# Optimization experiments

Measured on AMD Instinct MI355X. Metric: run time of the kernel, lower is better.

Reference implementation:

```python
import jax, jax.numpy as jnp
import numpy as np

N = 100000   # nodes
E = 3200000  # edges (avg degree 32)
G = 512      # graphs in batch
F_IN = 10
H = 30


def setup_inputs() -> dict:
    key = jax.random.key(0)
    ks = jax.random.split(key, 14)
    x = jax.random.normal(ks[0], (N, F_IN), dtype=jnp.float32)
    edge_index = jax.random.randint(ks[1], (2, E), 0, N, dtype=jnp.int64)
    batch = jnp.sort(jax.random.randint(ks[2], (N,), 0, G, dtype=jnp.int64))
    edge_weights = jnp.ones((E,), dtype=jnp.float32)
    s = 0.1
    W1 = jax.random.normal(ks[3], (F_IN, H), jnp.float32) * s
    b1 = jnp.zeros((H,), jnp.float32)
    W2 = jax.random.normal(ks[4], (H, H), jnp.float32) * s
    b2 = jnp.zeros((H,), jnp.float32)
    W3 = jax.random.normal(ks[5], (H, H), jnp.float32) * s
    b3 = jnp.zeros((H,), jnp.float32)
    LW1 = jax.random.normal(ks[6], (H, 10), jnp.float32) * s
    Lb1 = jnp.zeros((10,), jnp.float32)
    LW2 = jax.random.normal(ks[7], (10, 2), jnp.float32) * s
    Lb2 = jnp.zeros((2,), jnp.float32)
    return dict(x=x, edge_index=edge_index, batch=batch, edge_weights=edge_weights,
                W1=W1, b1=b1, W2=W2, b2=b2, W3=W3, b3=b3,
                LW1=LW1, Lb1=Lb1, LW2=LW2, Lb2=Lb2)


def reference(x, edge_index, batch, edge_weights, W1, b1, W2, b2, W3, b3, LW1, Lb1, LW2, Lb2):
    n = x.shape[0]
    row, col = edge_index[0], edge_index[1]
    # PyG gcn_norm: add self-loops with weight 1, symmetric normalization
    loop = jnp.arange(n)
    row_f = jnp.concatenate([row, loop])
    col_f = jnp.concatenate([col, loop])
    w_f = jnp.concatenate([edge_weights, jnp.ones((n,), edge_weights.dtype)])
    deg = jax.ops.segment_sum(w_f, col_f, num_segments=n)
    dis = jnp.where(deg > 0, jax.lax.rsqrt(jnp.where(deg > 0, deg, 1.0)), 0.0)
    norm = dis[row_f] * w_f * dis[col_f]  # [E+N]

    def gcn(h, W, b):
        h = h @ W  # [N, out]
        agg = jax.ops.segment_sum(norm[:, None] * h[row_f], col_f, num_segments=n)
        return agg + b

    h = jax.nn.relu(gcn(x, W1, b1))
    h = jax.nn.relu(gcn(h, W2, b2))
    h = jax.nn.relu(gcn(h, W3, b3))  # embedding [N, 30]
    pooled = jax.ops.segment_max(h, batch, num_segments=G)  # [G, 30]
    out = jax.nn.relu(pooled @ LW1 + Lb1) @ LW2 + Lb2  # [G, 2]
    return out
```

## Files before the change

kernel.cpp:

```cpp
#include <hip/hip_runtime.h>
#include <hip/hip_bf16.h>


#define WG 256
#define CAP 9216
#define T_EDGES 16384

__global__ void k_init(int* bcur, float* pooled, int nb16, int pooledN) {
    int i = blockIdx.x * blockDim.x + threadIdx.x;
    if (i < nb16) bcur[i] = 0;
    if (i < pooledN) pooled[i] = 0.0f;
}

__global__ __launch_bounds__(1024)
void k_bucket(const int* __restrict__ row, const int* __restrict__ col,
              const float* __restrict__ w,
              int* bcur, int2* __restrict__ buck, int E, int NB) {
    __shared__ int hist[512];
    __shared__ int base[512];
    int tid = threadIdx.x;
    for (int i = tid; i < NB; i += 1024) hist[i] = 0;
    __syncthreads();
    int start = blockIdx.x * T_EDGES;
    int end = min(start + T_EDGES, E);
    for (int i = start + tid; i < end; i += 1024)
        atomicAdd(&hist[col[i] >> 8], 1);
    __syncthreads();
    for (int i = tid; i < NB; i += 1024) {
        int h = hist[i];
        base[i] = (h > 0) ? atomicAdd(&bcur[i * 16], h) : 0;
        hist[i] = 0;
    }
    __syncthreads();
    for (int i = start + tid; i < end; i += 1024) {
        int c = col[i];
        int b = c >> 8;
        int off = atomicAdd(&hist[b], 1);
        int pos = base[b] + off;
        if (pos < CAP) {
            int2 pk;
            pk.x = (c & 255) | (row[i] << 8);
            pk.y = __float_as_int(w[i]);
            buck[(size_t)b * CAP + pos] = pk;
        }
    }
}

__global__ __launch_bounds__(1024)
void k_fuse(const int* __restrict__ bcur, const int2* __restrict__ buck,
            const float* __restrict__ x,
            float* __restrict__ dis, int* __restrict__ ptr,
            int2* __restrict__ csr, float* __restrict__ xp, int N, int NB) {
    __shared__ int lc[256];
    __shared__ float lw[256];
    __shared__ int sh[256];
    __shared__ int cur[256];
    __shared__ int sb[512];
    __shared__ float ds[256];
    int b = blockIdx.x;
    int tid = threadIdx.x;
    if (tid < 512) sb[tid] = (tid < NB) ? min(bcur[tid * 16], CAP) : 0;
    if (tid < 256) { lc[tid] = 0; lw[tid] = 0.0f; }
    __syncthreads();
    for (int off = 1; off < 512; off <<= 1) {
        int v = (tid < 512 && tid >= off) ? sb[tid - off] : 0;
        __syncthreads();
        if (tid < 512) sb[tid] += v;
        __syncthreads();
    }
    int m = min(bcur[b * 16], CAP);
    int bbase = sb[b] - m;
    if (b == 0 && tid == 0) ptr[N] = sb[511];
    const int2* bp = buck + (size_t)b * CAP;
    for (int i = tid; i < m; i += 1024) {
        int2 pk = bp[i];
        int lcol = pk.x & 255;
        atomicAdd(&lc[lcol], 1);
        atomicAdd(&lw[lcol], __int_as_float(pk.y));
    }
    __syncthreads();
    int lcnt = 0;
    if (tid < 256) { lcnt = lc[tid]; sh[tid] = lcnt; }
    __syncthreads();
    for (int off = 1; off < 256; off <<= 1) {
        int t = (tid >= off && tid < 256) ? sh[tid - off] : 0;
        __syncthreads();
        if (tid < 256) sh[tid] += t;
        __syncthreads();
    }
    int node = (b << 8) + tid;
    if (tid < 256) {
        int base = bbase + sh[tid] - lcnt;
        cur[tid] = base;
        float d = 1.0f + lw[tid];
        float dv = (d > 0.0f) ? (1.0f / sqrtf(d)) : 0.0f;
        ds[tid] = dv;
        if (node < N) {
            ptr[node] = base;
            dis[node] = dv;
        }
    }
    __syncthreads();
    for (int i = tid; i < m; i += 1024) {
        int2 pk = bp[i];
        int lcol = pk.x & 255;
        int pos = atomicAdd(&cur[lcol], 1);
        int2 rec;
        rec.x = (int)(((unsigned)pk.x) >> 8);
        rec.y = pk.y;
        csr[pos] = rec;
    }
    for (int i = tid; i < 256 * 16; i += 1024) {
        int nl = i >> 4, f = i & 15;
        int nd = (b << 8) + nl;
        if (nd < N)
            xp[(size_t)nd * 16 + f] = (f < 10) ? ds[nl] * x[(size_t)nd * 10 + f] : 0.0f;
    }
}

__global__ void k_agg16(const float* __restrict__ xp, const float* __restrict__ dis,
                        const int* __restrict__ ptr, const int2* __restrict__ csr,
                        float* __restrict__ y, int n) {
    int wid = (blockIdx.x * blockDim.x + threadIdx.x) >> 6;
    int lane = threadIdx.x & 63;
    if (wid >= n) return;
    int f = lane & 15;
    int q = lane >> 4;
    int s = ptr[wid];
    int e = ptr[wid + 1];
    float acc = 0.0f;
    int i = s;
    int efull = s + ((e - s) & ~31);
    for (; i < efull; i += 32) {
        int idxv = 0; float nrmv = 0.0f;
        if (lane < 32) {
            int2 v = csr[i + lane];
            idxv = v.x;
            nrmv = __int_as_float(v.y);
        }
#pragma unroll
        for (int j = 0; j < 8; j++) {
            int sl = 4 * j + q;
            int r = __shfl(idxv, sl, 64);
            float w = __shfl(nrmv, sl, 64);
            acc += w * xp[(size_t)r * 16 + f];
        }
    }
    int rem = e - i;
    if (rem > 0) {
        int idxv = 0; float nrmv = 0.0f;
        if (lane < rem) {
            int2 v = csr[i + lane];
            idxv = v.x;
            nrmv = __int_as_float(v.y);
        }
        for (int t = 0; t < rem; t += 8) {
#pragma unroll
            for (int j = 0; j < 2; j++) {
                int sl = t + 4 * j + q;
                int r = __shfl(idxv, sl, 64);
                float w = __shfl(nrmv, sl, 64);
                acc += w * xp[(size_t)r * 16 + f];
            }
        }
    }
    acc += __shfl_xor(acc, 16, 64);
    acc += __shfl_xor(acc, 32, 64);
    float dc = dis[wid];
    float r = dc * (acc + xp[(size_t)wid * 16 + f]);
    if (lane < 16) y[(size_t)wid * 16 + f] = r;
}

__global__ __launch_bounds__(256)
void k_lin1(const float* __restrict__ y, const float* __restrict__ W1,
            const float* __restrict__ b1, const float* __restrict__ W2,
            const float* __restrict__ dis, float* __restrict__ out, int n) {
    __shared__ float W1s[10 * 32];
    __shared__ float W2s[30 * 32];
    __shared__ float b1s[32];
    __shared__ float ys[8][16];
    __shared__ float hs[8][32];
    int tid = threadIdx.x;
    for (int i = tid; i < 10 * 32; i += 256) { int k = i >> 5, f = i & 31; W1s[i] = (f < 30) ? W1[k * 30 + f] : 0.0f; }
    for (int i = tid; i < 30 * 32; i += 256) { int k = i >> 5, f = i & 31; W2s[i] = (f < 30) ? W2[k * 30 + f] : 0.0f; }
    if (tid < 32) b1s[tid] = (tid < 30) ? b1[tid] : 0.0f;
    int n8 = tid >> 5, f = tid & 31;
    int node = blockIdx.x * 8 + n8;
    __syncthreads();
    if (node < n && f < 16) ys[n8][f] = y[(size_t)node * 16 + f];
    __syncthreads();
    if (node < n) {
        float h = b1s[f];
#pragma unroll
        for (int k = 0; k < 10; k++) h += ys[n8][k] * W1s[k * 32 + f];
        h = fmaxf(h, 0.0f);
        if (f >= 30) h = 0.0f;
        hs[n8][f] = h;
    }
    __syncthreads();
    if (node < n) {
        float o = 0.0f;
#pragma unroll
        for (int k = 0; k < 30; k++) o += hs[n8][k] * W2s[k * 32 + f];
        out[(size_t)node * 32 + f] = o * dis[node];
    }
}

__global__ void k_matmul30(const float* __restrict__ in,
                           const float* __restrict__ W, const float* __restrict__ dis,
                           float* __restrict__ out, int n) {
    __shared__ float Ws[30 * 30];
    for (int idx = threadIdx.x; idx < 30 * 30; idx += blockDim.x) Ws[idx] = W[idx];
    __syncthreads();
    int gid = blockIdx.x * blockDim.x + threadIdx.x;
    int node = gid >> 5;
    int f = gid & 31;
    if (node < n) {
        float acc = 0.0f;
        if (f < 30) {
            const float* ip = in + (size_t)node * 32;
#pragma unroll
            for (int k = 0; k < 30; k++) acc += ip[k] * Ws[k * 30 + f];
            acc *= dis[node];
        }
        out[(size_t)node * 32 + f] = acc;
    }
}

__global__ void k_agg(const float* __restrict__ hw, const float* __restrict__ dis,
                      const int* __restrict__ ptr, const int2* __restrict__ csr,
                      const float* __restrict__ bias,
                      float* __restrict__ out, int n) {
    int wid = (blockIdx.x * blockDim.x + threadIdx.x) >> 6;
    int lane = threadIdx.x & 63;
    if (wid >= n) return;
    int f = lane & 31;
    int half = lane >> 5;
    int s = ptr[wid];
    int e = ptr[wid + 1];
    float acc = 0.0f;
    int i = s;
    int efull = s + ((e - s) & ~31);
    for (; i < efull; i += 32) {
        int idxv = 0; float nrmv = 0.0f;
        if (lane < 32) {
            int2 v = csr[i + lane];
            idxv = v.x;
            nrmv = __int_as_float(v.y);
        }
#pragma unroll
        for (int j = 0; j < 16; j++) {
            int sl = 2 * j + half;
            int r = __shfl(idxv, sl, 64);
            float w = __shfl(nrmv, sl, 64);
            acc += w * hw[(size_t)r * 32 + f];
        }
    }
    int rem = e - i;
    if (rem > 0) {
        int idxv = 0; float nrmv = 0.0f;
        if (lane < rem) {
            int2 v = csr[i + lane];
            idxv = v.x;
            nrmv = __int_as_float(v.y);
        }
        for (int t = 0; t < rem; t += 8) {
#pragma unroll
            for (int j = 0; j < 4; j++) {
                int sl = t + 2 * j + half;
                int r = __shfl(idxv, sl, 64);
                float w = __shfl(nrmv, sl, 64);
                acc += w * hw[(size_t)r * 32 + f];
            }
        }
    }
    acc += __shfl_xor(acc, 32, 64);
    float dc = dis[wid];
    float r = dc * (acc + hw[(size_t)wid * 32 + f]);
    if (half == 0 && f < 30) {
        r += bias[f];
        out[(size_t)wid * 32 + f] = fmaxf(r, 0.0f);
    }
}

__global__ void k_pool(const float* __restrict__ h, const int* __restrict__ batch,
                       float* pooled, int n) {
    int gid = blockIdx.x * blockDim.x + threadIdx.x;
    int chunk = gid >> 5;
    int f = gid & 31;
    int n0 = chunk * 64;
    if (n0 >= n || f >= 30) return;
    int end = min(n0 + 64, n);
    int curg = batch[n0];
    float m = 0.0f;
    for (int i = n0; i < end; i++) {
        int g = batch[i];
        if (g != curg) {
            atomicMax((int*)&pooled[curg * 32 + f], __float_as_int(m));
            m = 0.0f;
            curg = g;
        }
        m = fmaxf(m, h[(size_t)i * 32 + f]);
    }
    atomicMax((int*)&pooled[curg * 32 + f], __float_as_int(m));
}

__global__ void k_mlp(const float* __restrict__ pooled,
                      const float* __restrict__ LW1, const float* __restrict__ Lb1,
                      const float* __restrict__ LW2, const float* __restrict__ Lb2,
                      float* __restrict__ out, int G) {
    int g = blockIdx.x * blockDim.x + threadIdx.x;
    if (g >= G) return;
    float p[30];
#pragma unroll
    for (int k = 0; k < 30; k++) p[k] = pooled[g * 32 + k];
    float o0 = Lb2[0], o1 = Lb2[1];
#pragma unroll
    for (int j = 0; j < 10; j++) {
        float hj = Lb1[j];
#pragma unroll
        for (int k = 0; k < 30; k++) hj += p[k] * LW1[k * 10 + j];
        hj = fmaxf(hj, 0.0f);
        o0 += hj * LW2[j * 2 + 0];
        o1 += hj * LW2[j * 2 + 1];
    }
    out[g * 2 + 0] = o0;
    out[g * 2 + 1] = o1;
}

extern "C" void kernel_launch(void* const* d_in, const int* in_sizes, int n_in,
                              void* d_out, int out_size, void* d_ws, size_t ws_size,
                              hipStream_t stream) {
    const float* x     = (const float*)d_in[0];
    const int*   ei    = (const int*)d_in[1];
    const int*   batch = (const int*)d_in[2];
    const float* ew    = (const float*)d_in[3];
    const float* W1 = (const float*)d_in[4];  const float* b1  = (const float*)d_in[5];
    const float* W2 = (const float*)d_in[6];  const float* b2  = (const float*)d_in[7];
    const float* W3 = (const float*)d_in[8];  const float* b3  = (const float*)d_in[9];
    const float* LW1 = (const float*)d_in[10]; const float* Lb1 = (const float*)d_in[11];
    const float* LW2 = (const float*)d_in[12]; const float* Lb2 = (const float*)d_in[13];
    float* out = (float*)d_out;

    const int N = in_sizes[2];
    const int E = in_sizes[3];
    const int G = out_size / 2;
    const int* row = ei;
    const int* col = ei + E;

    const int NB = (N + 255) >> 8;

    char* p = (char*)d_ws;
    auto carve = [&](size_t bytes) -> void* {
        void* r = (void*)p;
        p += (bytes + 255) & ~(size_t)255;
        return r;
    };
    int*   ptr       = (int*)carve((size_t)(N + 1) * 4);
    float* dis       = (float*)carve((size_t)N * 4);
    int*   bcur      = (int*)carve((size_t)NB * 16 * 4);
    float* xp        = (float*)carve((size_t)N * 16 * 4);
    int2*  csr       = (int2*)carve((size_t)E * 8);
    size_t buckBytes = (size_t)NB * CAP * 8;
    size_t featBytes = (size_t)N * 32 * 4 * 2;
    char*  regionA   = (char*)carve(buckBytes > featBytes ? buckBytes : featBytes);
    int2*  buck      = (int2*)regionA;
    float* bufA      = (float*)regionA;
    float* y16       = (float*)regionA;
    float* bufB      = (float*)(regionA + (size_t)N * 32 * 4);
    float* pooled    = (float*)carve((size_t)G * 32 * 4);

    int initN = (NB * 16 > G * 32) ? NB * 16 : G * 32;

    k_init<<<(initN + WG - 1) / WG, WG, 0, stream>>>(bcur, pooled, NB * 16, G * 32);
    k_bucket<<<(E + T_EDGES - 1) / T_EDGES, 1024, 0, stream>>>(row, col, ew, bcur, buck, E, NB);
    k_fuse<<<NB, 1024, 0, stream>>>(bcur, buck, x, dis, ptr, csr, xp, N, NB);

    int agg_grid = (int)(((size_t)N * 64 + WG - 1) / WG);
    int mm_grid  = (int)(((size_t)N * 32 + WG - 1) / WG);

    k_agg16<<<agg_grid, WG, 0, stream>>>(xp, dis, ptr, csr, y16, N);
    k_lin1<<<(N + 7) / 8, 256, 0, stream>>>(y16, W1, b1, W2, dis, bufB, N);
    k_agg<<<agg_grid, WG, 0, stream>>>(bufB, dis, ptr, csr, b2, bufA, N);
    k_matmul30<<<mm_grid, WG, 0, stream>>>(bufA, W3, dis, bufB, N);
    k_agg<<<agg_grid, WG, 0, stream>>>(bufB, dis, ptr, csr, b3, bufA, N);

    int pool_grid = (int)((((size_t)(N + 63) / 64) * 32 + WG - 1) / WG);
    k_pool<<<pool_grid, WG, 0, stream>>>(bufA, batch, pooled, N);
    k_mlp<<<(G + WG - 1) / WG, WG, 0, stream>>>(pooled, LW1, Lb1, LW2, Lb2, out, G);
}
```

Baseline: 429.7 us.

## Use per-wave histograms in edge bucketing and split feature staging into own kernel

The bucketing kernel now keeps a separate shared-memory histogram for each wave and caches column indices in registers. This cuts LDS atomic contention and avoids reloading col in the scatter pass. Per-wave prefix offsets are computed for each bin before the single global atomic reservation. The scaling of x by dis moves out of k_fuse into a separate elementwise kernel, which adds one launch but shortens the fused CSR-build kernel. The register array and the larger shared footprint may reduce occupancy.

```diff
diff --git a/kernel.cpp b/kernel.cpp
--- a/kernel.cpp
+++ b/kernel.cpp
@@ -5,6 +5,7 @@
 #define WG 256
 #define CAP 9216
 #define T_EDGES 16384
+#define NBINS 392
 
 __global__ void k_init(int* bcur, float* pooled, int nb16, int pooledN) {
     int i = blockIdx.x * blockDim.x + threadIdx.x;
@@ -16,47 +17,60 @@
 void k_bucket(const int* __restrict__ row, const int* __restrict__ col,
               const float* __restrict__ w,
               int* bcur, int2* __restrict__ buck, int E, int NB) {
-    __shared__ int hist[512];
-    __shared__ int base[512];
+    __shared__ int whist[16 * NBINS];
     int tid = threadIdx.x;
-    for (int i = tid; i < NB; i += 1024) hist[i] = 0;
+    int wave = tid >> 6;
+    for (int i = tid; i < 16 * NBINS; i += 1024) whist[i] = 0;
     __syncthreads();
     int start = blockIdx.x * T_EDGES;
-    int end = min(start + T_EDGES, E);
-    for (int i = start + tid; i < end; i += 1024)
-        atomicAdd(&hist[col[i] >> 8], 1);
-    __syncthreads();
-    for (int i = tid; i < NB; i += 1024) {
-        int h = hist[i];
-        base[i] = (h > 0) ? atomicAdd(&bcur[i * 16], h) : 0;
-        hist[i] = 0;
-    }
-    __syncthreads();
-    for (int i = start + tid; i < end; i += 1024) {
-        int c = col[i];
-        int b = c >> 8;
-        int off = atomicAdd(&hist[b], 1);
-        int pos = base[b] + off;
-        if (pos < CAP) {
-            int2 pk;
-            pk.x = (c & 255) | (row[i] << 8);
-            pk.y = __float_as_int(w[i]);
-            buck[(size_t)b * CAP + pos] = pk;
+    int cols[16];
+#pragma unroll
+    for (int j = 0; j < 16; j++) {
+        int i = start + tid + j * 1024;
+        int c = (i < E) ? col[i] : -1;
+        cols[j] = c;
+        if (c >= 0) atomicAdd(&whist[wave * NBINS + (c >> 8)], 1);
+    }
+    __syncthreads();
+    for (int b = tid; b < NB; b += 1024) {
+        int run = 0;
+#pragma unroll
+        for (int wv = 0; wv < 16; wv++) {
+            int c = whist[wv * NBINS + b];
+            whist[wv * NBINS + b] = run;
+            run += c;
+        }
+        int base = (run > 0) ? atomicAdd(&bcur[b * 16], run) : 0;
+#pragma unroll
+        for (int wv = 0; wv < 16; wv++) whist[wv * NBINS + b] += base;
+    }
+    __syncthreads();
+#pragma unroll
+    for (int j = 0; j < 16; j++) {
+        int i = start + tid + j * 1024;
+        int c = cols[j];
+        if (c >= 0) {
+            int b = c >> 8;
+            int pos = atomicAdd(&whist[wave * NBINS + b], 1);
+            if (pos < CAP) {
+                int2 pk;
+                pk.x = (c & 255) | (row[i] << 8);
+                pk.y = __float_as_int(w[i]);
+                buck[(size_t)b * CAP + pos] = pk;
+            }
         }
     }
 }
 
 __global__ __launch_bounds__(1024)
 void k_fuse(const int* __restrict__ bcur, const int2* __restrict__ buck,
-            const float* __restrict__ x,
             float* __restrict__ dis, int* __restrict__ ptr,
-            int2* __restrict__ csr, float* __restrict__ xp, int N, int NB) {
+            int2* __restrict__ csr, int N, int NB) {
     __shared__ int lc[256];
     __shared__ float lw[256];
     __shared__ int sh[256];
     __shared__ int cur[256];
     __shared__ int sb[512];
-    __shared__ float ds[256];
     int b = blockIdx.x;
     int tid = threadIdx.x;
     if (tid < 512) sb[tid] = (tid < NB) ? min(bcur[tid * 16], CAP) : 0;
@@ -92,12 +106,10 @@
     if (tid < 256) {
         int base = bbase + sh[tid] - lcnt;
         cur[tid] = base;
-        float d = 1.0f + lw[tid];
-        float dv = (d > 0.0f) ? (1.0f / sqrtf(d)) : 0.0f;
-        ds[tid] = dv;
         if (node < N) {
             ptr[node] = base;
-            dis[node] = dv;
+            float d = 1.0f + lw[tid];
+            dis[node] = (d > 0.0f) ? (1.0f / sqrtf(d)) : 0.0f;
         }
     }
     __syncthreads();
@@ -110,12 +122,14 @@
         rec.y = pk.y;
         csr[pos] = rec;
     }
-    for (int i = tid; i < 256 * 16; i += 1024) {
-        int nl = i >> 4, f = i & 15;
-        int nd = (b << 8) + nl;
-        if (nd < N)
-            xp[(size_t)nd * 16 + f] = (f < 10) ? ds[nl] * x[(size_t)nd * 10 + f] : 0.0f;
-    }
+}
+
+__global__ void k_stage(const float* __restrict__ x, const float* __restrict__ dis,
+                        float* __restrict__ xp, int n) {
+    int gid = blockIdx.x * blockDim.x + threadIdx.x;
+    int node = gid >> 4, f = gid & 15;
+    if (node < n)
+        xp[(size_t)node * 16 + f] = (f < 10) ? dis[node] * x[(size_t)node * 10 + f] : 0.0f;
 }
 
 __global__ void k_agg16(const float* __restrict__ xp, const float* __restrict__ dis,
@@ -374,11 +388,12 @@
 
     k_init<<<(initN + WG - 1) / WG, WG, 0, stream>>>(bcur, pooled, NB * 16, G * 32);
     k_bucket<<<(E + T_EDGES - 1) / T_EDGES, 1024, 0, stream>>>(row, col, ew, bcur, buck, E, NB);
-    k_fuse<<<NB, 1024, 0, stream>>>(bcur, buck, x, dis, ptr, csr, xp, N, NB);
+    k_fuse<<<NB, 1024, 0, stream>>>(bcur, buck, dis, ptr, csr, N, NB);
 
     int agg_grid = (int)(((size_t)N * 64 + WG - 1) / WG);
     int mm_grid  = (int)(((size_t)N * 32 + WG - 1) / WG);
 
+    k_stage<<<(int)(((size_t)N * 16 + WG - 1) / WG), WG, 0, stream>>>(x, dis, xp, N);
     k_agg16<<<agg_grid, WG, 0, stream>>>(xp, dis, ptr, csr, y16, N);
     k_lin1<<<(N + 7) / 8, 256, 0, stream>>>(y16, W1, b1, W2, dis, bufB, N);
     k_agg<<<agg_grid, WG, 0, stream>>>(bufB, dis, ptr, csr, b2, bufA, N);
```

Measured after the change: 428.0 us. About the same (-0.4%).
